# Kernel tuning notes

Hardware: AMD Instinct MI355X
Metric: run time of the kernel (lower is better)

The kernel has to match this reference:

```python
import jax, jax.numpy as jnp
import numpy as np

N, C, D, G, FC0, FC1, TOPK = 1024, 2, 1024, 16, 64, 16, 10
DG = D // G  # 64, per-group dim for WQ/WK
OPG = D // G  # 64, conv output channels per group (dim[2]=1024, groups=16)


def setup_inputs() -> dict:
    key = jax.random.key(0)
    ks = jax.random.split(key, 11)
    s = 0.02
    return {
        "f_a": jax.random.normal(ks[0], (N, C, D), jnp.float32),
        "position_embedding": jax.random.uniform(ks[1], (C, N, N, FC0), jnp.float32),
        "iou": jax.random.uniform(ks[2], (C, N, N), jnp.float32),
        "WG_w": jax.random.normal(ks[3], (FC1, FC0), jnp.float32) * s,
        "WG_b": jnp.zeros((FC1,), jnp.float32),
        "WK_w": jax.random.normal(ks[4], (D, D), jnp.float32) * s,
        "WK_b": jnp.zeros((D,), jnp.float32),
        "WQ_w": jax.random.normal(ks[5], (D, D), jnp.float32) * s,
        "WQ_b": jnp.zeros((D,), jnp.float32),
        "conv_w": jax.random.normal(ks[6], (D, D), jnp.float32) * s,  # [out=1024, in_per_group=1024] (1x1 kernel squeezed)
        "conv_b": jnp.zeros((D,), jnp.float32),
    }


def reference(f_a, position_embedding, iou, WG_w, WG_b, WK_w, WK_b, WQ_w, WQ_b, conv_w, conv_b):
    n = f_a.shape[0]
    k = min(n, TOPK)
    fa = jnp.transpose(f_a, (1, 0, 2))  # [C, N, D]

    # geometric bias: relu(Linear) -> [C, N, N, G] -> [C, G, N, N]
    w_g = jax.nn.relu(jnp.einsum('cmne,oe->cmno', position_embedding, WG_w) + WG_b)
    w_g = jnp.transpose(w_g, (0, 3, 1, 2))  # [C, G, N, N]

    # multi-head Q/K with per-group dim DG
    w_k = (jnp.einsum('cnd,ed->cne', fa, WK_w) + WK_b).reshape(C, n, G, DG)
    w_q = (jnp.einsum('cnd,ed->cne', fa, WQ_w) + WQ_b).reshape(C, n, G, DG)
    aff = jnp.einsum('cngd,cmgd->cgnm', w_q, w_k) / jnp.sqrt(jnp.float32(DG))  # [C, G, N, N]

    # iou_method == 'b': iou >= 1e-6 -> log(1)=0, else log(1e-6)
    log_iou = jnp.where(iou >= 1e-6, jnp.float32(0.0), jnp.log(jnp.float32(1e-6)))[:, None, :, :]

    w_mn = jnp.log(jnp.clip(w_g, 1e-6, None)) + aff + log_iou  # [C, G, N, N]

    # topk -> softmax over topk -> scatter back into dense [C, G, N, N]
    vals, idx = jax.lax.top_k(w_mn, k)
    soft = jax.nn.softmax(vals, axis=-1)
    ci = jnp.arange(C)[:, None, None, None]
    gi = jnp.arange(G)[None, :, None, None]
    ri = jnp.arange(n)[None, None, :, None]
    attn = jnp.zeros_like(w_mn).at[ci, gi, ri, idx].set(soft)

    # sparse attention-weighted aggregation of values
    out = jnp.einsum('cgnm,cmd->cgnd', attn, fa)  # [C, G, N, D]

    # grouped 1x1 conv: group g maps its D input channels to OPG output channels
    Wr = conv_w.reshape(G, OPG, D)  # [g, o_local, i]
    y = jnp.einsum('goi,cgni->ncgo', Wr, out).reshape(n, C, G * OPG) + conv_b  # [N, C, 1024]
    return y
```

## Files before the change

kernel.cpp:

```cpp
#include <hip/hip_runtime.h>
#include <math.h>

#define NT 1024
#define CD 2
#define DD 1024
#define GG 16
#define LOG1E6 -13.8155105579642740f
#define NEG_BIG -1e30f

typedef short bf16x8 __attribute__((ext_vector_type(8)));
typedef float f32x4  __attribute__((ext_vector_type(4)));

__device__ __forceinline__ unsigned short bf16_rne(float x) {
    unsigned int u = __float_as_uint(x);
    unsigned int r = (u + 0x7fffu + ((u >> 16) & 1u)) >> 16;
    return (unsigned short)r;
}

__device__ __forceinline__ void split3_8(const float* v, bf16x8& h, bf16x8& m, bf16x8& l) {
    #pragma unroll
    for (int e = 0; e < 8; ++e) {
        const float x = v[e];
        const unsigned short hb = bf16_rne(x);
        const float hf = __uint_as_float((unsigned int)hb << 16);
        const float r1 = x - hf;
        const unsigned short mb = bf16_rne(r1);
        const float mf = __uint_as_float((unsigned int)mb << 16);
        const float r2 = r1 - mf;
        const unsigned short lb = bf16_rne(r2);
        h[e] = (short)hb; m[e] = (short)mb; l[e] = (short)lb;
    }
}

__global__ __launch_bounds__(256) void k0_split(
    const float* __restrict__ fa, const float* __restrict__ Wq,
    const float* __restrict__ Wk, const float* __restrict__ Wc,
    unsigned short* __restrict__ Fh, unsigned short* __restrict__ Fm, unsigned short* __restrict__ Fl,
    unsigned short* __restrict__ WQh, unsigned short* __restrict__ WQm, unsigned short* __restrict__ WQl,
    unsigned short* __restrict__ WKh, unsigned short* __restrict__ WKm, unsigned short* __restrict__ WKl,
    unsigned short* __restrict__ WCh, unsigned short* __restrict__ WCm, unsigned short* __restrict__ WCl)
{
    const int reg = blockIdx.y;
    const float* src = (reg == 0) ? fa : (reg == 1) ? Wq : (reg == 2) ? Wk : Wc;
    unsigned short* dh = (reg == 0) ? Fh : (reg == 1) ? WQh : (reg == 2) ? WKh : WCh;
    unsigned short* dm = (reg == 0) ? Fm : (reg == 1) ? WQm : (reg == 2) ? WKm : WCm;
    unsigned short* dl = (reg == 0) ? Fl : (reg == 1) ? WQl : (reg == 2) ? WKl : WCl;
    const int nv = (reg == 0) ? (1 << 19) : (1 << 18);

    for (int v = blockIdx.x * 256 + threadIdx.x; v < nv; v += gridDim.x * 256) {
        float4 x4 = *(const float4*)&src[(size_t)v * 4];
        float xv[4] = {x4.x, x4.y, x4.z, x4.w};
        ushort4 h4, m4, l4;
        unsigned short hv[4], mv[4], lv[4];
        #pragma unroll
        for (int q = 0; q < 4; ++q) {
            const float x = xv[q];
            const unsigned short hb = bf16_rne(x);
            const float hf = __uint_as_float((unsigned int)hb << 16);
            const float r1 = x - hf;
            const unsigned short mb = bf16_rne(r1);
            const float mf = __uint_as_float((unsigned int)mb << 16);
            const unsigned short lb = bf16_rne(r1 - mf);
            hv[q] = hb; mv[q] = mb; lv[q] = lb;
        }
        h4.x = hv[0]; h4.y = hv[1]; h4.z = hv[2]; h4.w = hv[3];
        m4.x = mv[0]; m4.y = mv[1]; m4.z = mv[2]; m4.w = mv[3];
        l4.x = lv[0]; l4.y = lv[1]; l4.z = lv[2]; l4.w = lv[3];
        *(ushort4*)&dh[(size_t)v * 4] = h4;
        *(ushort4*)&dm[(size_t)v * 4] = m4;
        *(ushort4*)&dl[(size_t)v * 4] = l4;
    }
}

__global__ __launch_bounds__(256) void k1_mfma(
    const unsigned short* __restrict__ Fh, const unsigned short* __restrict__ Fm,
    const unsigned short* __restrict__ Fl,
    const unsigned short* __restrict__ WQh, const unsigned short* __restrict__ WQm,
    const unsigned short* __restrict__ WQl,
    const unsigned short* __restrict__ WKh, const unsigned short* __restrict__ WKm,
    const unsigned short* __restrict__ WKl,
    const unsigned short* __restrict__ WCh, const unsigned short* __restrict__ WCm,
    const unsigned short* __restrict__ WCl,
    const float* __restrict__ bq, const float* __restrict__ bk, const float* __restrict__ bc,
    float* __restrict__ Qo, float* __restrict__ Ko, float* __restrict__ Vo)
{
    const int et = blockIdx.x, rt = blockIdx.y, z = blockIdx.z;
    const unsigned short* Wh = (z == 0) ? WQh : (z == 1) ? WKh : WCh;
    const unsigned short* Wm = (z == 0) ? WQm : (z == 1) ? WKm : WCm;
    const unsigned short* Wl = (z == 0) ? WQl : (z == 1) ? WKl : WCl;
    const float* bb = (z == 0) ? bq : (z == 1) ? bk : bc;
    float* Out      = (z == 0) ? Qo : (z == 1) ? Ko : Vo;

    const int c  = rt >> 3;
    const int n0 = (rt & 7) * 128;
    const int r0 = rt * 128;
    const int e0 = et * 64;

    __shared__ unsigned short Ah[128][36], Am[128][36], Al[128][36];
    __shared__ unsigned short Bh[64][36],  Bm[64][36],  Bl[64][36];

    const int t    = threadIdx.x;
    const int wave = t >> 6, lane = t & 63;
    const int wr   = wave >> 1, wc = wave & 1;
    const int lrow = lane & 15, lk = lane >> 4;

    f32x4 acc[4][2];
    #pragma unroll
    for (int m = 0; m < 4; ++m)
        #pragma unroll
        for (int n = 0; n < 2; ++n) acc[m][n] = (f32x4){0.f, 0.f, 0.f, 0.f};

    for (int kt = 0; kt < 32; ++kt) {
        const int kb = kt * 32;
        #pragma unroll
        for (int p = 0; p < 2; ++p) {
            const int task = t + p * 256;
            const int row = task >> 2, seg = task & 3;
            const size_t gs = ((size_t)((n0 + row) * CD + c)) * DD + kb + seg * 8;
            *(uint4*)&Ah[row][seg * 8] = *(const uint4*)&Fh[gs];
            *(uint4*)&Am[row][seg * 8] = *(const uint4*)&Fm[gs];
            *(uint4*)&Al[row][seg * 8] = *(const uint4*)&Fl[gs];
        }
        {
            const int row = t >> 2, seg = t & 3;
            const size_t gs = ((size_t)(e0 + row)) * DD + kb + seg * 8;
            *(uint4*)&Bh[row][seg * 8] = *(const uint4*)&Wh[gs];
            *(uint4*)&Bm[row][seg * 8] = *(const uint4*)&Wm[gs];
            *(uint4*)&Bl[row][seg * 8] = *(const uint4*)&Wl[gs];
        }
        __syncthreads();
        {
            bf16x8 ah[4], am[4], al[4], bh[2], bm[2], bl[2];
            #pragma unroll
            for (int m = 0; m < 4; ++m) {
                const int row = wr * 64 + m * 16 + lrow;
                ah[m] = *(const bf16x8*)&Ah[row][lk * 8];
                am[m] = *(const bf16x8*)&Am[row][lk * 8];
                al[m] = *(const bf16x8*)&Al[row][lk * 8];
            }
            #pragma unroll
            for (int n = 0; n < 2; ++n) {
                const int row = wc * 32 + n * 16 + lrow;
                bh[n] = *(const bf16x8*)&Bh[row][lk * 8];
                bm[n] = *(const bf16x8*)&Bm[row][lk * 8];
                bl[n] = *(const bf16x8*)&Bl[row][lk * 8];
            }
            #pragma unroll
            for (int m = 0; m < 4; ++m)
                #pragma unroll
                for (int n = 0; n < 2; ++n) {
                    acc[m][n] = __builtin_amdgcn_mfma_f32_16x16x32_bf16(al[m], bh[n], acc[m][n], 0, 0, 0);
                    acc[m][n] = __builtin_amdgcn_mfma_f32_16x16x32_bf16(ah[m], bl[n], acc[m][n], 0, 0, 0);
                    acc[m][n] = __builtin_amdgcn_mfma_f32_16x16x32_bf16(am[m], bm[n], acc[m][n], 0, 0, 0);
                    acc[m][n] = __builtin_amdgcn_mfma_f32_16x16x32_bf16(am[m], bh[n], acc[m][n], 0, 0, 0);
                    acc[m][n] = __builtin_amdgcn_mfma_f32_16x16x32_bf16(ah[m], bm[n], acc[m][n], 0, 0, 0);
                    acc[m][n] = __builtin_amdgcn_mfma_f32_16x16x32_bf16(ah[m], bh[n], acc[m][n], 0, 0, 0);
                }
        }
        __syncthreads();
    }
    #pragma unroll
    for (int n = 0; n < 2; ++n) {
        const int e = e0 + wc * 32 + n * 16 + lrow;
        const float bias = bb[e];
        #pragma unroll
        for (int m = 0; m < 4; ++m) {
            const int r = r0 + wr * 64 + m * 16 + lk * 4;
            #pragma unroll
            for (int q = 0; q < 4; ++q)
                Out[((size_t)(r + q)) * DD + e] = acc[m][n][q] + bias;
        }
    }
}

__global__ __launch_bounds__(256) void k2a_aff(
    const float* __restrict__ Q, const float* __restrict__ Km,
    float* __restrict__ aff)
{
    const int jt = blockIdx.x, it = blockIdx.y, cg = blockIdx.z;
    const int c = cg >> 4, g = cg & 15;
    __shared__ float Ql[64][68];
    __shared__ float Kl[64][68];
    const int t = threadIdx.x;
    const int dd = t & 15, rr = t >> 4;
    const int i0 = it * 64, j0 = jt * 64;
    #pragma unroll
    for (int p = 0; p < 4; ++p) {
        const int row = rr + p * 16;
        float4 q4 = *(const float4*)&Q[((size_t)(c * NT + i0 + row)) * DD + g * 64 + dd * 4];
        Ql[dd*4+0][row] = q4.x; Ql[dd*4+1][row] = q4.y;
        Ql[dd*4+2][row] = q4.z; Ql[dd*4+3][row] = q4.w;
        float4 k4 = *(const float4*)&Km[((size_t)(c * NT + j0 + row)) * DD + g * 64 + dd * 4];
        Kl[dd*4+0][row] = k4.x; Kl[dd*4+1][row] = k4.y;
        Kl[dd*4+2][row] = k4.z; Kl[dd*4+3][row] = k4.w;
    }
    __syncthreads();
    const int tx = t & 15, ty = t >> 4;
    float acc[4][4];
    #pragma unroll
    for (int a = 0; a < 4; ++a)
        #pragma unroll
        for (int b = 0; b < 4; ++b) acc[a][b] = 0.f;
    #pragma unroll 8
    for (int d = 0; d < 64; ++d) {
        float4 q4 = *(const float4*)&Ql[d][ty * 4];
        float4 k4 = *(const float4*)&Kl[d][tx * 4];
        float qv[4] = {q4.x, q4.y, q4.z, q4.w};
        float kv[4] = {k4.x, k4.y, k4.z, k4.w};
        #pragma unroll
        for (int a = 0; a < 4; ++a)
            #pragma unroll
            for (int b = 0; b < 4; ++b) acc[a][b] += qv[a] * kv[b];
    }
    #pragma unroll
    for (int a = 0; a < 4; ++a) {
        float4 o;
        o.x = acc[a][0] * 0.125f; o.y = acc[a][1] * 0.125f;
        o.z = acc[a][2] * 0.125f; o.w = acc[a][3] * 0.125f;
        *(float4*)&aff[(((size_t)(c * GG + g)) * NT + i0 + ty * 4 + a) * NT + j0 + tx * 4] = o;
    }
}

__global__ __launch_bounds__(256, 4) void k3_scan(
    const float* __restrict__ pe, const float* __restrict__ iou,
    const float* __restrict__ WGw, const float* __restrict__ WGb,
    const float* __restrict__ aff,
    float* __restrict__ cv, int* __restrict__ ci)
{
    const int ch = blockIdx.x;
    const int it = blockIdx.y;
    const int c  = blockIdx.z;
    const int i0 = it * 8;

    __shared__ float wgl[8][16][33];
    __shared__ float ios[8][33];

    const int t = threadIdx.x;
    const int wave = t >> 6, lane = t & 63;
    const int lg = lane & 15, lk = lane >> 4;
    const int p_i = t >> 5, jq = t & 31;
    const int s_i = t >> 5, s_g = (t >> 1) & 15, s_h = t & 1;

    bf16x8 bh[2], bm[2], bl[2];
    #pragma unroll
    for (int kp = 0; kp < 2; ++kp) {
        float w8[8];
        float4 w0 = *(const float4*)&WGw[lg * 64 + kp * 32 + lk * 8];
        float4 w1 = *(const float4*)&WGw[lg * 64 + kp * 32 + lk * 8 + 4];
        w8[0]=w0.x; w8[1]=w0.y; w8[2]=w0.z; w8[3]=w0.w;
        w8[4]=w1.x; w8[5]=w1.y; w8[6]=w1.z; w8[7]=w1.w;
        split3_8(w8, bh[kp], bm[kp], bl[kp]);
    }
    const float bias = WGb[lg];

    float tv[10]; int tidx[10];
    #pragma unroll
    for (int q = 0; q < 10; ++q) { tv[q] = NEG_BIG; tidx[q] = 0; }

    for (int s = 0; s < 8; ++s) {
        const int j0 = ch * 256 + s * 32;
        {
            const float ia = iou[((size_t)c * NT + (i0 + p_i)) * NT + j0 + jq];
            ios[p_i][jq] = (ia >= 1e-6f) ? 0.f : LOG1E6;
        }
        #pragma unroll 1
        for (int rtt = 0; rtt < 4; ++rtt) {
            const int rt = wave * 4 + rtt;
            const int ib = rt >> 1;
            const int jb = (rt & 1) * 16;
            const float* pr = &pe[(((size_t)c * NT + (i0 + ib)) * NT + (j0 + jb + lg)) * 64];
            f32x4 acc = {0.f, 0.f, 0.f, 0.f};
            #pragma unroll
            for (int kp = 0; kp < 2; ++kp) {
                float a8[8];
                float4 v0 = *(const float4*)&pr[kp * 32 + lk * 8];
                float4 v1 = *(const float4*)&pr[kp * 32 + lk * 8 + 4];
                a8[0]=v0.x; a8[1]=v0.y; a8[2]=v0.z; a8[3]=v0.w;
                a8[4]=v1.x; a8[5]=v1.y; a8[6]=v1.z; a8[7]=v1.w;
                bf16x8 ah, am, al;
                split3_8(a8, ah, am, al);
                acc = __builtin_amdgcn_mfma_f32_16x16x32_bf16(al, bh[kp], acc, 0, 0, 0);
                acc = __builtin_amdgcn_mfma_f32_16x16x32_bf16(ah, bl[kp], acc, 0, 0, 0);
                acc = __builtin_amdgcn_mfma_f32_16x16x32_bf16(am, bm[kp], acc, 0, 0, 0);
                acc = __builtin_amdgcn_mfma_f32_16x16x32_bf16(am, bh[kp], acc, 0, 0, 0);
                acc = __builtin_amdgcn_mfma_f32_16x16x32_bf16(ah, bm[kp], acc, 0, 0, 0);
                acc = __builtin_amdgcn_mfma_f32_16x16x32_bf16(ah, bh[kp], acc, 0, 0, 0);
            }
            #pragma unroll
            for (int q = 0; q < 4; ++q) {
                const float v = acc[q] + bias;
                wgl[ib][lg][jb + lk * 4 + q] = (v > 1e-6f) ? __logf(v) : LOG1E6;
            }
        }
        __syncthreads();
        {
            const float* ar = &aff[(((size_t)(c * GG + s_g)) * NT + (i0 + s_i)) * NT + j0 + s_h * 16];
            const float* wl = &wgl[s_i][s_g][s_h * 16];
            const float* il = &ios[s_i][s_h * 16];
            #pragma unroll
            for (int j4 = 0; j4 < 16; j4 += 4) {
                float4 a4 = *(const float4*)&ar[j4];
                float av[4] = {a4.x, a4.y, a4.z, a4.w};
                #pragma unroll
                for (int q = 0; q < 4; ++q) {
                    const float val = wl[j4 + q] + av[q] + il[j4 + q];
                    if (val > tv[0]) {
                        const int ix = j0 + s_h * 16 + j4 + q;
                        #pragma unroll
                        for (int sl = 0; sl < 10; ++sl) {
                            const bool up   = (sl < 9) ? (val > tv[sl + 1]) : false;
                            const bool here = (val > tv[sl]);
                            const float ntv = up ? tv[sl + 1] : (here ? val : tv[sl]);
                            const int   nti = up ? tidx[sl + 1] : (here ? ix : tidx[sl]);
                            tv[sl] = ntv; tidx[sl] = nti;
                        }
                    }
                }
            }
        }
        __syncthreads();
    }

    float* mv = &wgl[0][0][0];
    int*   mi = (int*)(mv + 1280);
    const int pair = t >> 1;
    if (s_h == 1) {
        #pragma unroll
        for (int q = 0; q < 10; ++q) { mv[pair * 10 + q] = tv[q]; mi[pair * 10 + q] = tidx[q]; }
    }
    __syncthreads();
    if (s_h == 0) {
        for (int q = 9; q >= 0; --q) {
            const float val = mv[pair * 10 + q];
            const int   ix  = mi[pair * 10 + q];
            if (val > tv[0]) {
                #pragma unroll
                for (int sl = 0; sl < 10; ++sl) {
                    const bool up   = (sl < 9) ? (val > tv[sl + 1]) : false;
                    const bool here = (val > tv[sl]);
                    const float ntv = up ? tv[sl + 1] : (here ? val : tv[sl]);
                    const int   nti = up ? tidx[sl + 1] : (here ? ix : tidx[sl]);
                    tv[sl] = ntv; tidx[sl] = nti;
                }
            }
        }
        const size_t base = ((((size_t)c * NT + (i0 + s_i)) * GG + s_g) * 4 + ch) * 10;
        #pragma unroll
        for (int q = 0; q < 10; ++q) { cv[base + q] = tv[q]; ci[base + q] = tidx[q]; }
    }
}

__global__ __launch_bounds__(256) void k2b2_fin(
    const float* __restrict__ cv, const int* __restrict__ ci,
    const float* __restrict__ V, float* __restrict__ y)
{
    const int w    = (blockIdx.x << 2) + (threadIdx.x >> 6);
    const int lane = threadIdx.x & 63;
    const int c = w >> 14;
    const int i = (w >> 4) & (NT - 1);
    const int g = w & 15;

    float tv[10]; int tidx[10];
    #pragma unroll
    for (int q = 0; q < 10; ++q) { tv[q] = NEG_BIG; tidx[q] = 0; }

    const size_t base = (size_t)w * 40;
    for (int chn = 0; chn < 4; ++chn) {
        const float* cvp = &cv[base + chn * 10];
        const int*   cip = &ci[base + chn * 10];
        for (int q = 9; q >= 0; --q) {
            const float val = cvp[q];
            const int   ix  = cip[q];
            if (val > tv[0]) {
                #pragma unroll
                for (int sl = 0; sl < 10; ++sl) {
                    const bool up   = (sl < 9) ? (val > tv[sl + 1]) : false;
                    const bool here = (val > tv[sl]);
                    const float ntv = up ? tv[sl + 1] : (here ? val : tv[sl]);
                    const int   nti = up ? tidx[sl + 1] : (here ? ix : tidx[sl]);
                    tv[sl] = ntv; tidx[sl] = nti;
                }
            }
        }
    }
    const float m = tv[9];
    float wgt[10]; float sm = 0.f;
    #pragma unroll
    for (int q = 0; q < 10; ++q) { wgt[q] = __expf(tv[q] - m); sm += wgt[q]; }
    const float inv = 1.f / sm;
    float o = 0.f;
    #pragma unroll
    for (int q = 0; q < 10; ++q)
        o += (wgt[q] * inv) * V[((size_t)(c * NT + tidx[q])) * DD + g * 64 + lane];
    y[((size_t)i * CD + c) * DD + g * 64 + lane] = o;
}

extern "C" void kernel_launch(void* const* d_in, const int* in_sizes, int n_in,
                              void* d_out, int out_size, void* d_ws, size_t ws_size,
                              hipStream_t stream) {
    (void)in_sizes; (void)n_in; (void)out_size; (void)ws_size;
    const float* f_a = (const float*)d_in[0];
    const float* pe  = (const float*)d_in[1];
    const float* iou = (const float*)d_in[2];
    const float* WGw = (const float*)d_in[3];
    const float* WGb = (const float*)d_in[4];
    const float* WKw = (const float*)d_in[5];
    const float* WKb = (const float*)d_in[6];
    const float* WQw = (const float*)d_in[7];
    const float* WQb = (const float*)d_in[8];
    const float* Cw  = (const float*)d_in[9];
    const float* Cb  = (const float*)d_in[10];
    float* yout = (float*)d_out;

    float* ws  = (float*)d_ws;
    float* Q   = ws;
    float* Kp  = ws + (1u << 21);
    float* V   = ws + (2u << 21);
    float* aff = ws + (3u << 21);
    float* cv  = ws;
    int*   ci  = (int*)(ws + (1u << 21));
    unsigned short* sp = (unsigned short*)(ws + (3u << 21) + (1u << 25));
    const size_t FN = (size_t)CD * NT * DD;
    const size_t WN = (size_t)DD * DD / 1;
    unsigned short* Fh  = sp;
    unsigned short* Fm  = Fh + FN;
    unsigned short* Fl  = Fm + FN;
    unsigned short* WQh = Fl + FN;
    unsigned short* WQm = WQh + WN;
    unsigned short* WQl = WQm + WN;
    unsigned short* WKh = WQl + WN;
    unsigned short* WKm = WKh + WN;
    unsigned short* WKl = WKm + WN;
    unsigned short* WCh = WKl + WN;
    unsigned short* WCm = WCh + WN;
    unsigned short* WCl = WCm + WN;

    k0_split<<<dim3(512, 4), 256, 0, stream>>>(f_a, WQw, WKw, Cw,
        Fh, Fm, Fl, WQh, WQm, WQl, WKh, WKm, WKl, WCh, WCm, WCl);
    k1_mfma<<<dim3(16, 16, 3), 256, 0, stream>>>(
        Fh, Fm, Fl, WQh, WQm, WQl, WKh, WKm, WKl, WCh, WCm, WCl,
        WQb, WKb, Cb, Q, Kp, V);
    k2a_aff<<<dim3(16, 16, 32), 256, 0, stream>>>(Q, Kp, aff);
    k3_scan<<<dim3(4, 128, 2), 256, 0, stream>>>(pe, iou, WGw, WGb, aff, cv, ci);
    k2b2_fin<<<8192, 256, 0, stream>>>(cv, ci, V, yout);
}
```

Baseline: 426.3 us.

## Compute Q·K affinity with split-bf16 MFMA, emitting split Q/K from projection

The projection kernel now writes Q and K directly as three-way bf16 splits (hi/mid/lo) instead of fp32. The affinity kernel is rewritten to use 16x16x32 bf16 MFMA with six partial products, in place of scalar FP32 FMAs from shared memory. This moves the 2x16x1024x1024x64 affinity GEMM onto matrix cores, aiming to keep near-fp32 accuracy for the top-k selection. The cost is extra split arithmetic and scattered 2-byte stores in the projection epilogue, plus non-vectorised aff stores.

```diff
diff --git a/kernel.cpp b/kernel.cpp
--- a/kernel.cpp
+++ b/kernel.cpp
@@ -82,14 +82,18 @@
     const unsigned short* __restrict__ WCh, const unsigned short* __restrict__ WCm,
     const unsigned short* __restrict__ WCl,
     const float* __restrict__ bq, const float* __restrict__ bk, const float* __restrict__ bc,
-    float* __restrict__ Qo, float* __restrict__ Ko, float* __restrict__ Vo)
+    float* __restrict__ Vo,
+    unsigned short* __restrict__ QSh, unsigned short* __restrict__ QSm, unsigned short* __restrict__ QSl,
+    unsigned short* __restrict__ KSh, unsigned short* __restrict__ KSm, unsigned short* __restrict__ KSl)
 {
     const int et = blockIdx.x, rt = blockIdx.y, z = blockIdx.z;
     const unsigned short* Wh = (z == 0) ? WQh : (z == 1) ? WKh : WCh;
     const unsigned short* Wm = (z == 0) ? WQm : (z == 1) ? WKm : WCm;
     const unsigned short* Wl = (z == 0) ? WQl : (z == 1) ? WKl : WCl;
     const float* bb = (z == 0) ? bq : (z == 1) ? bk : bc;
-    float* Out      = (z == 0) ? Qo : (z == 1) ? Ko : Vo;
+    unsigned short* Sh = (z == 0) ? QSh : KSh;
+    unsigned short* Sm = (z == 0) ? QSm : KSm;
+    unsigned short* Sl = (z == 0) ? QSl : KSl;
 
     const int c  = rt >> 3;
     const int n0 = (rt & 7) * 128;
@@ -167,57 +171,104 @@
         for (int m = 0; m < 4; ++m) {
             const int r = r0 + wr * 64 + m * 16 + lk * 4;
             #pragma unroll
-            for (int q = 0; q < 4; ++q)
-                Out[((size_t)(r + q)) * DD + e] = acc[m][n][q] + bias;
-        }
-    }
-}
-
-__global__ __launch_bounds__(256) void k2a_aff(
-    const float* __restrict__ Q, const float* __restrict__ Km,
+            for (int q = 0; q < 4; ++q) {
+                const float val = acc[m][n][q] + bias;
+                const size_t idx = ((size_t)(r + q)) * DD + e;
+                if (z == 2) {
+                    Vo[idx] = val;
+                } else {
+                    const unsigned short hb = bf16_rne(val);
+                    const float hf = __uint_as_float((unsigned int)hb << 16);
+                    const float r1 = val - hf;
+                    const unsigned short mb = bf16_rne(r1);
+                    const float mf = __uint_as_float((unsigned int)mb << 16);
+                    const unsigned short lb = bf16_rne(r1 - mf);
+                    Sh[idx] = hb; Sm[idx] = mb; Sl[idx] = lb;
+                }
+            }
+        }
+    }
+}
+
+__global__ __launch_bounds__(256) void k2a_mfma(
+    const unsigned short* __restrict__ QSh, const unsigned short* __restrict__ QSm,
+    const unsigned short* __restrict__ QSl,
+    const unsigned short* __restrict__ KSh, const unsigned short* __restrict__ KSm,
+    const unsigned short* __restrict__ KSl,
     float* __restrict__ aff)
 {
     const int jt = blockIdx.x, it = blockIdx.y, cg = blockIdx.z;
     const int c = cg >> 4, g = cg & 15;
-    __shared__ float Ql[64][68];
-    __shared__ float Kl[64][68];
-    const int t = threadIdx.x;
-    const int dd = t & 15, rr = t >> 4;
     const int i0 = it * 64, j0 = jt * 64;
-    #pragma unroll
-    for (int p = 0; p < 4; ++p) {
-        const int row = rr + p * 16;
-        float4 q4 = *(const float4*)&Q[((size_t)(c * NT + i0 + row)) * DD + g * 64 + dd * 4];
-        Ql[dd*4+0][row] = q4.x; Ql[dd*4+1][row] = q4.y;
-        Ql[dd*4+2][row] = q4.z; Ql[dd*4+3][row] = q4.w;
-        float4 k4 = *(const float4*)&Km[((size_t)(c * NT + j0 + row)) * DD + g * 64 + dd * 4];
-        Kl[dd*4+0][row] = k4.x; Kl[dd*4+1][row] = k4.y;
-        Kl[dd*4+2][row] = k4.z; Kl[dd*4+3][row] = k4.w;
-    }
-    __syncthreads();
-    const int tx = t & 15, ty = t >> 4;
-    float acc[4][4];
-    #pragma unroll
-    for (int a = 0; a < 4; ++a)
-        #pragma unroll
-        for (int b = 0; b < 4; ++b) acc[a][b] = 0.f;
-    #pragma unroll 8
-    for (int d = 0; d < 64; ++d) {
-        float4 q4 = *(const float4*)&Ql[d][ty * 4];
-        float4 k4 = *(const float4*)&Kl[d][tx * 4];
-        float qv[4] = {q4.x, q4.y, q4.z, q4.w};
-        float kv[4] = {k4.x, k4.y, k4.z, k4.w};
-        #pragma unroll
-        for (int a = 0; a < 4; ++a)
-            #pragma unroll
-            for (int b = 0; b < 4; ++b) acc[a][b] += qv[a] * kv[b];
-    }
-    #pragma unroll
-    for (int a = 0; a < 4; ++a) {
-        float4 o;
-        o.x = acc[a][0] * 0.125f; o.y = acc[a][1] * 0.125f;
-        o.z = acc[a][2] * 0.125f; o.w = acc[a][3] * 0.125f;
-        *(float4*)&aff[(((size_t)(c * GG + g)) * NT + i0 + ty * 4 + a) * NT + j0 + tx * 4] = o;
+
+    __shared__ unsigned short Qh[64][36], Qm[64][36], Ql[64][36];
+    __shared__ unsigned short Kh[64][36], Km[64][36], Kl[64][36];
+
+    const int t    = threadIdx.x;
+    const int wave = t >> 6, lane = t & 63;
+    const int wr   = wave >> 1, wc = wave & 1;
+    const int lrow = lane & 15, lk = lane >> 4;
+
+    f32x4 acc[2][2];
+    #pragma unroll
+    for (int m = 0; m < 2; ++m)
+        #pragma unroll
+        for (int n = 0; n < 2; ++n) acc[m][n] = (f32x4){0.f, 0.f, 0.f, 0.f};
+
+    for (int kt = 0; kt < 2; ++kt) {
+        const int kb = g * 64 + kt * 32;
+        {
+            const int row = t >> 2, seg = t & 3;
+            const size_t qs = ((size_t)(c * NT + i0 + row)) * DD + kb + seg * 8;
+            *(uint4*)&Qh[row][seg * 8] = *(const uint4*)&QSh[qs];
+            *(uint4*)&Qm[row][seg * 8] = *(const uint4*)&QSm[qs];
+            *(uint4*)&Ql[row][seg * 8] = *(const uint4*)&QSl[qs];
+            const size_t ks = ((size_t)(c * NT + j0 + row)) * DD + kb + seg * 8;
+            *(uint4*)&Kh[row][seg * 8] = *(const uint4*)&KSh[ks];
+            *(uint4*)&Km[row][seg * 8] = *(const uint4*)&KSm[ks];
+            *(uint4*)&Kl[row][seg * 8] = *(const uint4*)&KSl[ks];
+        }
+        __syncthreads();
+        {
+            bf16x8 qh[2], qm[2], ql[2], kh[2], km[2], kl[2];
+            #pragma unroll
+            for (int m = 0; m < 2; ++m) {
+                const int row = wr * 32 + m * 16 + lrow;
+                qh[m] = *(const bf16x8*)&Qh[row][lk * 8];
+                qm[m] = *(const bf16x8*)&Qm[row][lk * 8];
+                ql[m] = *(const bf16x8*)&Ql[row][lk * 8];
+            }
+            #pragma unroll
+            for (int n = 0; n < 2; ++n) {
+                const int row = wc * 32 + n * 16 + lrow;
+                kh[n] = *(const bf16x8*)&Kh[row][lk * 8];
+                km[n] = *(const bf16x8*)&Km[row][lk * 8];
+                kl[n] = *(const bf16x8*)&Kl[row][lk * 8];
+            }
+            #pragma unroll
+            for (int m = 0; m < 2; ++m)
+                #pragma unroll
+                for (int n = 0; n < 2; ++n) {
+                    acc[m][n] = __builtin_amdgcn_mfma_f32_16x16x32_bf16(ql[m], kh[n], acc[m][n], 0, 0, 0);
+                    acc[m][n] = __builtin_amdgcn_mfma_f32_16x16x32_bf16(qh[m], kl[n], acc[m][n], 0, 0, 0);
+                    acc[m][n] = __builtin_amdgcn_mfma_f32_16x16x32_bf16(qm[m], km[n], acc[m][n], 0, 0, 0);
+                    acc[m][n] = __builtin_amdgcn_mfma_f32_16x16x32_bf16(qm[m], kh[n], acc[m][n], 0, 0, 0);
+                    acc[m][n] = __builtin_amdgcn_mfma_f32_16x16x32_bf16(qh[m], km[n], acc[m][n], 0, 0, 0);
+                    acc[m][n] = __builtin_amdgcn_mfma_f32_16x16x32_bf16(qh[m], kh[n], acc[m][n], 0, 0, 0);
+                }
+        }
+        __syncthreads();
+    }
+    #pragma unroll
+    for (int m = 0; m < 2; ++m) {
+        const int i = i0 + wr * 32 + m * 16 + lk * 4;
+        #pragma unroll
+        for (int n = 0; n < 2; ++n) {
+            const int j = j0 + wc * 32 + n * 16 + lrow;
+            #pragma unroll
+            for (int q = 0; q < 4; ++q)
+                aff[((size_t)cg * NT + i + q) * NT + j] = acc[m][n][q] * 0.125f;
+        }
     }
 }
 
@@ -413,15 +464,13 @@
     float* yout = (float*)d_out;
 
     float* ws  = (float*)d_ws;
-    float* Q   = ws;
-    float* Kp  = ws + (1u << 21);
     float* V   = ws + (2u << 21);
     float* aff = ws + (3u << 21);
     float* cv  = ws;
     int*   ci  = (int*)(ws + (1u << 21));
     unsigned short* sp = (unsigned short*)(ws + (3u << 21) + (1u << 25));
     const size_t FN = (size_t)CD * NT * DD;
-    const size_t WN = (size_t)DD * DD / 1;
+    const size_t WN = (size_t)DD * DD;
     unsigned short* Fh  = sp;
     unsigned short* Fm  = Fh + FN;
     unsigned short* Fl  = Fm + FN;
@@ -434,13 +483,19 @@
     unsigned short* WCh = WKl + WN;
     unsigned short* WCm = WCh + WN;
     unsigned short* WCl = WCm + WN;
+    unsigned short* QSh = WCl + WN;
+    unsigned short* QSm = QSh + FN;
+    unsigned short* QSl = QSm + FN;
+    unsigned short* KSh = QSl + FN;
+    unsigned short* KSm = KSh + FN;
+    unsigned short* KSl = KSm + FN;
 
     k0_split<<<dim3(512, 4), 256, 0, stream>>>(f_a, WQw, WKw, Cw,
         Fh, Fm, Fl, WQh, WQm, WQl, WKh, WKm, WKl, WCh, WCm, WCl);
     k1_mfma<<<dim3(16, 16, 3), 256, 0, stream>>>(
         Fh, Fm, Fl, WQh, WQm, WQl, WKh, WKm, WKl, WCh, WCm, WCl,
-        WQb, WKb, Cb, Q, Kp, V);
-    k2a_aff<<<dim3(16, 16, 32), 256, 0, stream>>>(Q, Kp, aff);
+        WQb, WKb, Cb, V, QSh, QSm, QSl, KSh, KSm, KSl);
+    k2a_mfma<<<dim3(16, 16, 32), 256, 0, stream>>>(QSh, QSm, QSl, KSh, KSm, KSl, aff);
     k3_scan<<<dim3(4, 128, 2), 256, 0, stream>>>(pe, iou, WGw, WGb, aff, cv, ci);
     k2b2_fin<<<8192, 256, 0, stream>>>(cv, ci, V, yout);
 }
```

After: 410.5 us. -3.7%, faster.
